# Kernel tuning notes

Measured on AMD Instinct MI355X. Metric: run time of the kernel, lower is better.

Reference implementation:

```python
import jax, jax.numpy as jnp
import numpy as np

H = 16        # num_attention_heads
KV = 4        # num_key_value_heads
HD = 128      # head_dim = hidden_size // H
ROPE_THETA = 10000.0


def _rotate_half(x):
    x1, x2 = jnp.split(x, 2, axis=-1)
    return jnp.concatenate([-x2, x1], axis=-1)


def _rope_cos_sin(seq_len, dtype):
    # inv_freq: (HD//2,), full rotary (partial_rotary_factor=1.0), attention_scaling=1.0
    inv_freq = 1.0 / (ROPE_THETA ** (jnp.arange(0, HD, 2, dtype=jnp.float32) / HD))
    pos = jnp.arange(seq_len, dtype=jnp.float32)
    freqs = pos[:, None] * inv_freq[None, :]              # (S, HD//2)
    emb = jnp.concatenate([freqs, freqs], axis=-1)        # (S, HD)
    # expansion_axis=2 -> broadcast over heads: (1, S, 1, HD)
    return (jnp.cos(emb)[None, :, None, :].astype(dtype),
            jnp.sin(emb)[None, :, None, :].astype(dtype))


def setup_inputs() -> dict:
    key = jax.random.key(0)
    k1, k2, k3, k4, k5 = jax.random.split(key, 5)
    B, S, D = 2, 2048, 2048
    hidden_states = jax.random.normal(k1, (B, S, D), dtype=jnp.float32)
    # causal mask, True = attend
    causal = jnp.tril(jnp.ones((S, S), dtype=bool))
    attention_mask = jnp.broadcast_to(causal[None, None, :, :], (B, 1, S, S))
    scale = 0.02
    Wq = jax.random.normal(k2, (D, H * HD), dtype=jnp.float32) * scale
    Wk = jax.random.normal(k3, (D, KV * HD), dtype=jnp.float32) * scale
    Wv = jax.random.normal(k4, (D, KV * HD), dtype=jnp.float32) * scale
    Wo = jax.random.normal(k5, (H, HD, D), dtype=jnp.float32) * scale
    return {"hidden_states": hidden_states, "attention_mask": attention_mask,
            "Wq": Wq, "Wk": Wk, "Wv": Wv, "Wo": Wo}


def reference(hidden_states, attention_mask, Wq, Wk, Wv, Wo):
    B, S, D = hidden_states.shape
    q = (hidden_states @ Wq).reshape(B, S, H, HD)   # bquh
    k = (hidden_states @ Wk).reshape(B, S, KV, HD)
    v = (hidden_states @ Wv).reshape(B, S, KV, HD)

    cos, sin = _rope_cos_sin(S, q.dtype)
    q = q * cos + _rotate_half(q) * sin
    k = k * cos + _rotate_half(k) * sin

    # GQA: repeat kv heads to match query heads
    groups = H // KV
    k = jnp.repeat(k, groups, axis=2)               # (B, S, H, HD)
    v = jnp.repeat(v, groups, axis=2)

    inv_norm = 1.0 / np.sqrt(HD)
    scores = jnp.einsum('bquh,bkuh->buqk', q, k) * inv_norm   # (B, H, Sq, Sk)
    scores = scores.astype(jnp.float32)
    neg = jnp.asarray(-1e9, dtype=jnp.float32)
    scores = jnp.where(attention_mask, scores, neg)
    probs = jax.nn.softmax(scores, axis=-1).astype(q.dtype)
    attn = jnp.einsum('buqk,bkuh->bquh', probs, v)             # (B, S, H, HD)
    out = jnp.einsum('bquh,uhm->bqm', attn, Wo)                # (B, S, D)
    return out
```

## Files before the change

### kernel.cpp

```cpp
#include <hip/hip_runtime.h>
#include <math.h>

namespace {

constexpr int B   = 2;
constexpr int S   = 2048;
constexpr int D   = 2048;
constexpr int NH  = 16;
constexpr int NKV = 4;
constexpr int HD  = 128;
constexpr int GRP = NH / NKV;

typedef __attribute__((ext_vector_type(8))) short  short8;
typedef __attribute__((ext_vector_type(4))) float  f32x4;
typedef unsigned short u16;

__device__ inline u16 f2bf(float f) {
    unsigned u = __float_as_uint(f);
    u = (u + 0x7FFFu + ((u >> 16) & 1u)) >> 16;
    return (u16)u;
}
__device__ inline float bf2f(u16 h) {
    return __uint_as_float((unsigned)h << 16);
}

__device__ __forceinline__ void gload_lds16(const void* g, void* l) {
    __builtin_amdgcn_global_load_lds(
        (const __attribute__((address_space(1))) unsigned int*)g,
        (__attribute__((address_space(3))) unsigned int*)l, 16, 0, 0);
}

__global__ __launch_bounds__(256)
void split_cast_kernel(const float* __restrict__ X, u16* __restrict__ H,
                       u16* __restrict__ L, int n4)
{
    const int idx = blockIdx.x * 256 + threadIdx.x;
    if (idx >= n4) return;
    const float4 v = reinterpret_cast<const float4*>(X)[idx];
    ushort4 h, l;
    h.x = f2bf(v.x); l.x = f2bf(v.x - bf2f(h.x));
    h.y = f2bf(v.y); l.y = f2bf(v.y - bf2f(h.y));
    h.z = f2bf(v.z); l.z = f2bf(v.z - bf2f(h.z));
    h.w = f2bf(v.w); l.w = f2bf(v.w - bf2f(h.w));
    reinterpret_cast<ushort4*>(H)[idx] = h;
    reinterpret_cast<ushort4*>(L)[idx] = l;
}

__global__ __launch_bounds__(256)
void wcast_t_kernel(const float* __restrict__ W, u16* __restrict__ Th,
                    u16* __restrict__ Tl, int Nw, int n_off)
{
    __shared__ u16 th[64][68];
    __shared__ u16 tl[64][68];
    const int t  = threadIdx.x;
    const int n0 = blockIdx.x * 64;
    const int k0 = blockIdx.y * 64;

#pragma unroll
    for (int i = 0; i < 4; ++i) {
        const int kr = (t >> 4) + i * 16;
        const int nc = (t & 15) * 4;
        const float4 v = *reinterpret_cast<const float4*>(
            &W[(size_t)(k0 + kr) * Nw + n0 + nc]);
        const u16 hx = f2bf(v.x), hy = f2bf(v.y), hz = f2bf(v.z), hw = f2bf(v.w);
        th[kr][nc + 0] = hx; tl[kr][nc + 0] = f2bf(v.x - bf2f(hx));
        th[kr][nc + 1] = hy; tl[kr][nc + 1] = f2bf(v.y - bf2f(hy));
        th[kr][nc + 2] = hz; tl[kr][nc + 2] = f2bf(v.z - bf2f(hz));
        th[kr][nc + 3] = hw; tl[kr][nc + 3] = f2bf(v.w - bf2f(hw));
    }
    __syncthreads();
#pragma unroll
    for (int i = 0; i < 4; ++i) {
        const int nr = (t >> 4) + i * 16;
        const int kc = (t & 15) * 4;
        ushort4 oh, ol;
        oh.x = th[kc + 0][nr]; ol.x = tl[kc + 0][nr];
        oh.y = th[kc + 1][nr]; ol.y = tl[kc + 1][nr];
        oh.z = th[kc + 2][nr]; ol.z = tl[kc + 2][nr];
        oh.w = th[kc + 3][nr]; ol.w = tl[kc + 3][nr];
        const size_t o = (size_t)(n_off + n0 + nr) * 2048 + k0 + kc;
        *reinterpret_cast<ushort4*>(&Th[o]) = oh;
        *reinterpret_cast<ushort4*>(&Tl[o]) = ol;
    }
}

__global__ __launch_bounds__(256)
void hgemm_hilo_kernel(const u16* __restrict__ Ah, const u16* __restrict__ Al,
                       const u16* __restrict__ Bth, const u16* __restrict__ Btl,
                       float* __restrict__ C, int M, int N, int K)
{
    __shared__ alignas(16) u16 AsH[4096];
    __shared__ alignas(16) u16 AsL[4096];
    __shared__ alignas(16) u16 BsH[4096];
    __shared__ alignas(16) u16 BsL[4096];

    const int t  = threadIdx.x;
    const int w  = t >> 6;
    const int l  = t & 63;
    const int lc = l & 15;
    const int kg = l >> 4;
    const int wr = w >> 1, wc = w & 1;

    const int m0 = blockIdx.y * 128;
    const int n0 = blockIdx.x * 128;

    const int srow = l >> 2;
    const int sblk = l & 3;

    f32x4 acc[4][4];
#pragma unroll
    for (int i = 0; i < 4; ++i)
#pragma unroll
        for (int j = 0; j < 4; ++j) acc[i][j] = (f32x4){0.f, 0.f, 0.f, 0.f};

    for (int k0 = 0; k0 < K; k0 += 32) {
#pragma unroll
        for (int i = 0; i < 2; ++i) {
            const int c   = i * 4 + w;
            const int row = c * 16 + srow;
            const int swb = sblk ^ ((row >> 1) & 3);
            const size_t ga = (size_t)(m0 + row) * K + k0 + swb * 8;
            const size_t gb = (size_t)(n0 + row) * K + k0 + swb * 8;
            gload_lds16(Ah  + ga, AsH + c * 512);
            gload_lds16(Al  + ga, AsL + c * 512);
            gload_lds16(Bth + gb, BsH + c * 512);
            gload_lds16(Btl + gb, BsL + c * 512);
        }
        __syncthreads();

        short8 fah[4], fal[4], fbh[4], fbl[4];
#pragma unroll
        for (int i = 0; i < 4; ++i) {
            const int ra = wr * 64 + i * 16 + lc;
            const int oa = ra * 32 + ((kg ^ ((ra >> 1) & 3)) * 8);
            fah[i] = *reinterpret_cast<const short8*>(&AsH[oa]);
            fal[i] = *reinterpret_cast<const short8*>(&AsL[oa]);
            const int rb = wc * 64 + i * 16 + lc;
            const int ob = rb * 32 + ((kg ^ ((rb >> 1) & 3)) * 8);
            fbh[i] = *reinterpret_cast<const short8*>(&BsH[ob]);
            fbl[i] = *reinterpret_cast<const short8*>(&BsL[ob]);
        }
#pragma unroll
        for (int i = 0; i < 4; ++i)
#pragma unroll
            for (int j = 0; j < 4; ++j) {
                acc[i][j] = __builtin_amdgcn_mfma_f32_16x16x32_bf16(
                    fal[i], fbh[j], acc[i][j], 0, 0, 0);
                acc[i][j] = __builtin_amdgcn_mfma_f32_16x16x32_bf16(
                    fah[i], fbl[j], acc[i][j], 0, 0, 0);
                acc[i][j] = __builtin_amdgcn_mfma_f32_16x16x32_bf16(
                    fah[i], fbh[j], acc[i][j], 0, 0, 0);
            }
        __syncthreads();
    }

#pragma unroll
    for (int i = 0; i < 4; ++i)
#pragma unroll
        for (int j = 0; j < 4; ++j)
#pragma unroll
            for (int r = 0; r < 4; ++r) {
                const int m = m0 + wr * 64 + i * 16 + kg * 4 + r;
                const int n = n0 + wc * 64 + j * 16 + lc;
                C[(size_t)m * N + n] = acc[i][j][r];
            }
}

__global__ __launch_bounds__(256)
void rope_cast_kernel(const float* __restrict__ X, int stride, int col_off,
                      u16* __restrict__ Yh, u16* __restrict__ Yl,
                      int n_heads, int total_pairs, float scale)
{
    const int idx = blockIdx.x * 256 + threadIdx.x;
    if (idx >= total_pairs) return;
    const int i    = idx & 63;
    const int rest = idx >> 6;
    const int head = rest % n_heads;
    const int row  = rest / n_heads;
    const int s    = row & (S - 1);
    const int b    = row >> 11;

    const float inv = expf(-9.2103403719761836f * (float)i * (1.0f / 64.0f));
    float sn, cs;
    sincosf((float)s * inv, &sn, &cs);

    const float* src = X + (size_t)row * stride + col_off + head * HD + i;
    const float x1 = src[0], x2 = src[64];
    const float y1 = (x1 * cs - x2 * sn) * scale;
    const float y2 = (x2 * cs + x1 * sn) * scale;

    const u16 h1 = f2bf(y1), h2 = f2bf(y2);
    const size_t o = ((size_t)(b * n_heads + head) * S + s) * HD + i;
    Yh[o] = h1;  Yh[o + 64] = h2;
    Yl[o]      = f2bf(y1 - bf2f(h1));
    Yl[o + 64] = f2bf(y2 - bf2f(h2));
}

__global__ __launch_bounds__(256)
void vcast_kernel(const float* __restrict__ V, int stride, int col_off,
                  u16* __restrict__ Yh, u16* __restrict__ Yl)
{
    __shared__ u16 th[64][68];
    __shared__ u16 tl[64][68];
    const int t  = threadIdx.x;
    const int s0 = blockIdx.x * 64, dv0 = blockIdx.y * 64;
    const int b  = blockIdx.z >> 2, u = blockIdx.z & 3;

#pragma unroll
    for (int i = 0; i < 4; ++i) {
        const int sr = (t >> 4) + i * 16;
        const int dc = (t & 15) * 4;
        const float4 v = *reinterpret_cast<const float4*>(
            &V[(size_t)(b * S + s0 + sr) * stride + col_off + u * HD + dv0 + dc]);
        const u16 hx = f2bf(v.x), hy = f2bf(v.y), hz = f2bf(v.z), hw = f2bf(v.w);
        th[sr][dc + 0] = hx; tl[sr][dc + 0] = f2bf(v.x - bf2f(hx));
        th[sr][dc + 1] = hy; tl[sr][dc + 1] = f2bf(v.y - bf2f(hy));
        th[sr][dc + 2] = hz; tl[sr][dc + 2] = f2bf(v.z - bf2f(hz));
        th[sr][dc + 3] = hw; tl[sr][dc + 3] = f2bf(v.w - bf2f(hw));
    }
    __syncthreads();
#pragma unroll
    for (int i = 0; i < 4; ++i) {
        const int dr = (t >> 4) + i * 16;
        const int sc = (t & 15) * 4;
        ushort4 oh, ol;
        oh.x = th[sc + 0][dr]; ol.x = tl[sc + 0][dr];
        oh.y = th[sc + 1][dr]; ol.y = tl[sc + 1][dr];
        oh.z = th[sc + 2][dr]; ol.z = tl[sc + 2][dr];
        oh.w = th[sc + 3][dr]; ol.w = tl[sc + 3][dr];
        const size_t o = ((size_t)(b * NKV + u) * HD + dv0 + dr) * S + s0 + sc;
        *reinterpret_cast<ushort4*>(&Yh[o]) = oh;
        *reinterpret_cast<ushort4*>(&Yl[o]) = ol;
    }
}

constexpr int QTILE = 64, KT = 32;

__global__ __launch_bounds__(256)
void flash_mfma_kernel(const u16* __restrict__ Qh, const u16* __restrict__ Ql,
                       const u16* __restrict__ Kh, const u16* __restrict__ Kl,
                       const u16* __restrict__ Vh, const u16* __restrict__ Vl,
                       u16* __restrict__ Oh, u16* __restrict__ Ol)
{
    __shared__ alignas(16) u16 smem[23552];
    u16* KsH = smem;
    u16* KsL = smem + 4096;
    u16* VtH = smem + 8192;
    u16* VtL = smem + 13312;
    u16* PH  = smem + 18432;
    u16* PL  = smem + 20992;

    const int t  = threadIdx.x;
    const int w  = t >> 6;
    const int ln = t & 63;
    const int lg = ln >> 4;
    const int lc = ln & 15;

    const int qt = (int)gridDim.x - 1 - (int)blockIdx.x;
    const int q0 = qt * QTILE;
    const int bh = blockIdx.y;
    const int b  = bh / NH, h = bh % NH, u = h / GRP;

    const size_t qbase = (size_t)(b * NH + h) * S * HD;
    const size_t kbase = (size_t)(b * NKV + u) * S * HD;
    const size_t vbase = (size_t)(b * NKV + u) * HD * S;

    {
        u16* QsH = smem;
        u16* QsL = smem + 8192;
#pragma unroll
        for (int i = 0; i < 4; ++i) {
            const int r = (t >> 4) + i * 16;
            const int blk = t & 15;
            const size_t src = qbase + (size_t)(q0 + r) * HD + blk * 8;
            const int dst = r * 128 + ((blk ^ (r & 7)) * 8);
            *reinterpret_cast<short8*>(&QsH[dst]) =
                *reinterpret_cast<const short8*>(&Qh[src]);
            *reinterpret_cast<short8*>(&QsL[dst]) =
                *reinterpret_cast<const short8*>(&Ql[src]);
        }
        __syncthreads();
    }
    short8 qah[4], qal[4];
#pragma unroll
    for (int ks = 0; ks < 4; ++ks) {
        const int qr = w * 16 + lc;
        const int off = qr * 128 + (((ks * 4 + lg) ^ (qr & 7)) * 8);
        qah[ks] = *reinterpret_cast<const short8*>(&smem[off]);
        qal[ks] = *reinterpret_cast<const short8*>(&smem[8192 + off]);
    }
    __syncthreads();

    f32x4 o[8];
#pragma unroll
    for (int i = 0; i < 8; ++i) o[i] = (f32x4){0.f, 0.f, 0.f, 0.f};
    float m_run[4] = {-1e30f, -1e30f, -1e30f, -1e30f};
    float l_run[4] = {0.f, 0.f, 0.f, 0.f};

    u16* PwH = PH + w * 640;
    u16* PwL = PL + w * 640;
    const int qw0 = q0 + w * 16;
    const int nkt = q0 / KT + 2;

    const int sr_k = t >> 4;
    const int sb_k = t & 15;
    const int sr_v = t >> 2;
    const int sb_v = t & 3;
    const int dKsw = (sb_k ^ (sr_k & 7)) * 8;
    const int dK0  = sr_k * 128 + dKsw;
    const int dK1  = (sr_k + 16) * 128 + dKsw;
    const int dV0  = sr_v * 40 + sb_v * 8;
    const int dV1  = (sr_v + 64) * 40 + sb_v * 8;

    short8 stg[8];
#define LOADTILE(K0)                                                          \
    {                                                                         \
        const size_t ksrc = kbase + (size_t)((K0) + sr_k) * HD + sb_k * 8;    \
        stg[0] = *reinterpret_cast<const short8*>(&Kh[ksrc]);                 \
        stg[1] = *reinterpret_cast<const short8*>(&Kh[ksrc + 16 * HD]);       \
        stg[2] = *reinterpret_cast<const short8*>(&Kl[ksrc]);                 \
        stg[3] = *reinterpret_cast<const short8*>(&Kl[ksrc + 16 * HD]);       \
        const size_t vsrc = vbase + (size_t)sr_v * S + (K0) + sb_v * 8;       \
        stg[4] = *reinterpret_cast<const short8*>(&Vh[vsrc]);                 \
        stg[5] = *reinterpret_cast<const short8*>(&Vh[vsrc + (size_t)64 * S]);\
        stg[6] = *reinterpret_cast<const short8*>(&Vl[vsrc]);                 \
        stg[7] = *reinterpret_cast<const short8*>(&Vl[vsrc + (size_t)64 * S]);\
    }

    LOADTILE(0);

    for (int kt = 0; kt < nkt; ++kt) {
        const int k0 = kt * KT;
        *reinterpret_cast<short8*>(&KsH[dK0]) = stg[0];
        *reinterpret_cast<short8*>(&KsH[dK1]) = stg[1];
        *reinterpret_cast<short8*>(&KsL[dK0]) = stg[2];
        *reinterpret_cast<short8*>(&KsL[dK1]) = stg[3];
        *reinterpret_cast<short8*>(&VtH[dV0]) = stg[4];
        *reinterpret_cast<short8*>(&VtH[dV1]) = stg[5];
        *reinterpret_cast<short8*>(&VtL[dV0]) = stg[6];
        *reinterpret_cast<short8*>(&VtL[dV1]) = stg[7];
        __syncthreads();

        if (kt + 1 < nkt) LOADTILE(k0 + KT);

        if (k0 <= qw0 + 15) {
            f32x4 a0 = {0.f, 0.f, 0.f, 0.f}, a1 = {0.f, 0.f, 0.f, 0.f};
            __builtin_amdgcn_s_setprio(1);
#pragma unroll
            for (int ks = 0; ks < 4; ++ks) {
                const int r0 = lc, r1 = 16 + lc;
                const int o0b = r0 * 128 + (((ks * 4 + lg) ^ (r0 & 7)) * 8);
                const int o1b = r1 * 128 + (((ks * 4 + lg) ^ (r1 & 7)) * 8);
                const short8 kb0h = *reinterpret_cast<const short8*>(&KsH[o0b]);
                const short8 kb0l = *reinterpret_cast<const short8*>(&KsL[o0b]);
                const short8 kb1h = *reinterpret_cast<const short8*>(&KsH[o1b]);
                const short8 kb1l = *reinterpret_cast<const short8*>(&KsL[o1b]);
                a0 = __builtin_amdgcn_mfma_f32_16x16x32_bf16(qal[ks], kb0h, a0, 0, 0, 0);
                a0 = __builtin_amdgcn_mfma_f32_16x16x32_bf16(qah[ks], kb0l, a0, 0, 0, 0);
                a0 = __builtin_amdgcn_mfma_f32_16x16x32_bf16(qah[ks], kb0h, a0, 0, 0, 0);
                a1 = __builtin_amdgcn_mfma_f32_16x16x32_bf16(qal[ks], kb1h, a1, 0, 0, 0);
                a1 = __builtin_amdgcn_mfma_f32_16x16x32_bf16(qah[ks], kb1l, a1, 0, 0, 0);
                a1 = __builtin_amdgcn_mfma_f32_16x16x32_bf16(qah[ks], kb1h, a1, 0, 0, 0);
            }
            __builtin_amdgcn_s_setprio(0);

            float s0v[4], s1v[4], mx[4];
            const bool need_mask = (k0 + KT - 1 > qw0);
#pragma unroll
            for (int r = 0; r < 4; ++r) {
                float s0 = a0[r], s1 = a1[r];
                const int qg = qw0 + lg * 4 + r;
                if (need_mask) {
                    if (k0 + lc > qg)      s0 = -1e30f;
                    if (k0 + 16 + lc > qg) s1 = -1e30f;
                }
                s0v[r] = s0; s1v[r] = s1;
                mx[r] = fmaxf(s0, s1);
            }
#pragma unroll
            for (int off = 1; off < 16; off <<= 1)
#pragma unroll
                for (int r = 0; r < 4; ++r)
                    mx[r] = fmaxf(mx[r], __shfl_xor(mx[r], off, 64));

            bool grow = false;
#pragma unroll
            for (int r = 0; r < 4; ++r) grow = grow || (mx[r] > m_run[r] + 8.0f);
            const bool resc_needed = __any((int)grow);

            float mn[4], rsc[4];
#pragma unroll
            for (int r = 0; r < 4; ++r) {
                mn[r]  = resc_needed ? fmaxf(m_run[r], mx[r]) : m_run[r];
                rsc[r] = resc_needed ? __expf(m_run[r] - mn[r]) : 1.0f;
            }
            float p0[4], p1[4], rs[4];
#pragma unroll
            for (int r = 0; r < 4; ++r) {
                p0[r] = __expf(s0v[r] - mn[r]);
                p1[r] = __expf(s1v[r] - mn[r]);
                rs[r] = p0[r] + p1[r];
            }
#pragma unroll
            for (int off = 1; off < 16; off <<= 1)
#pragma unroll
                for (int r = 0; r < 4; ++r)
                    rs[r] += __shfl_xor(rs[r], off, 64);
#pragma unroll
            for (int r = 0; r < 4; ++r) {
                l_run[r] = l_run[r] * rsc[r] + rs[r];
                m_run[r] = mn[r];
            }
            if (resc_needed) {
#pragma unroll
                for (int nt = 0; nt < 8; ++nt)
#pragma unroll
                    for (int r = 0; r < 4; ++r) o[nt][r] *= rsc[r];
            }
#pragma unroll
            for (int r = 0; r < 4; ++r) {
                const u16 p0h = f2bf(p0[r]);
                const u16 p1h = f2bf(p1[r]);
                const int row = (lg * 4 + r) * 40;
                PwH[row + lc]      = p0h;
                PwH[row + 16 + lc] = p1h;
                PwL[row + lc]      = f2bf(p0[r] - bf2f(p0h));
                PwL[row + 16 + lc] = f2bf(p1[r] - bf2f(p1h));
            }
            asm volatile("s_waitcnt lgkmcnt(0)" ::: "memory");

            const short8 pah = *reinterpret_cast<const short8*>(&PwH[lc * 40 + lg * 8]);
            const short8 pal = *reinterpret_cast<const short8*>(&PwL[lc * 40 + lg * 8]);
            __builtin_amdgcn_s_setprio(1);
#pragma unroll
            for (int nt = 0; nt < 8; ++nt) {
                const int dvo = (nt * 16 + lc) * 40 + lg * 8;
                const short8 vbh = *reinterpret_cast<const short8*>(&VtH[dvo]);
                const short8 vbl = *reinterpret_cast<const short8*>(&VtL[dvo]);
                o[nt] = __builtin_amdgcn_mfma_f32_16x16x32_bf16(pal, vbh, o[nt], 0, 0, 0);
                o[nt] = __builtin_amdgcn_mfma_f32_16x16x32_bf16(pah, vbl, o[nt], 0, 0, 0);
                o[nt] = __builtin_amdgcn_mfma_f32_16x16x32_bf16(pah, vbh, o[nt], 0, 0, 0);
            }
            __builtin_amdgcn_s_setprio(0);
        }
        __syncthreads();
    }
#undef LOADTILE

    float invl[4];
#pragma unroll
    for (int r = 0; r < 4; ++r) invl[r] = 1.f / l_run[r];
#pragma unroll
    for (int nt = 0; nt < 8; ++nt) {
#pragma unroll
        for (int r = 0; r < 4; ++r) {
            const float v = o[nt][r] * invl[r];
            const size_t off =
                (size_t)(b * S + qw0 + lg * 4 + r) * (NH * HD) + h * HD + nt * 16 + lc;
            const u16 hv = f2bf(v);
            Oh[off] = hv;
            Ol[off] = f2bf(v - bf2f(hv));
        }
    }
}

}

extern "C" void kernel_launch(void* const* d_in, const int* in_sizes, int n_in,
                              void* d_out, int out_size, void* d_ws, size_t ws_size,
                              hipStream_t stream)
{
    const float* hidden = (const float*)d_in[0];
    const float* Wq = (const float*)d_in[2];
    const float* Wk = (const float*)d_in[3];
    const float* Wv = (const float*)d_in[4];
    const float* Wo = (const float*)d_in[5];
    float* out = (float*)d_out;

    char* wsb = (char*)d_ws;
    u16*   hid_hi  = (u16*)(wsb);
    u16*   hid_lo  = (u16*)(wsb + 16777216);
    float* qkv_f   = (float*)(wsb + 33554432);
    u16*   k_hi    = (u16*)(wsb + 83886080);
    u16*   k_lo    = (u16*)(wsb + 88080384);
    u16*   v_hi    = (u16*)(wsb + 92274688);
    u16*   v_lo    = (u16*)(wsb + 96468992);
    u16*   wT_hi   = (u16*)(wsb + 100663296);
    u16*   wT_lo   = (u16*)(wsb + 113246208);
    u16* q_hi    = hid_hi;
    u16* q_lo    = hid_lo;
    u16* attn_hi = (u16*)(wsb + 33554432);
    u16* attn_lo = (u16*)(wsb + 50331648);
    u16* woT_hi  = wT_hi;
    u16* woT_lo  = wT_lo;

    const dim3 blk(256);

    split_cast_kernel<<<dim3(8192), blk, 0, stream>>>(hidden, hid_hi, hid_lo, 2097152);
    wcast_t_kernel<<<dim3(32, 32), blk, 0, stream>>>(Wq, wT_hi, wT_lo, 2048, 0);
    wcast_t_kernel<<<dim3(8, 32),  blk, 0, stream>>>(Wk, wT_hi, wT_lo, 512, 2048);
    wcast_t_kernel<<<dim3(8, 32),  blk, 0, stream>>>(Wv, wT_hi, wT_lo, 512, 2560);
    hgemm_hilo_kernel<<<dim3(24, 32), blk, 0, stream>>>(
        hid_hi, hid_lo, wT_hi, wT_lo, qkv_f, 4096, 3072, 2048);
    wcast_t_kernel<<<dim3(32, 32), blk, 0, stream>>>(Wo, woT_hi, woT_lo, 2048, 0);
    const int qpairs = 4096 * NH * 64;
    const int kpairs = 4096 * NKV * 64;
    rope_cast_kernel<<<dim3(qpairs / 256), blk, 0, stream>>>(
        qkv_f, 3072, 0, q_hi, q_lo, NH, qpairs, 0.08838834764831845f);
    rope_cast_kernel<<<dim3(kpairs / 256), blk, 0, stream>>>(
        qkv_f, 3072, 2048, k_hi, k_lo, NKV, kpairs, 1.0f);
    vcast_kernel<<<dim3(32, 2, 8), blk, 0, stream>>>(
        qkv_f, 3072, 2560, v_hi, v_lo);
    flash_mfma_kernel<<<dim3(S / QTILE, B * NH), blk, 0, stream>>>(
        q_hi, q_lo, k_hi, k_lo, v_hi, v_lo, attn_hi, attn_lo);
    hgemm_hilo_kernel<<<dim3(16, 32), blk, 0, stream>>>(
        attn_hi, attn_lo, woT_hi, woT_lo, out, 4096, 2048, 2048);
}
```

Before: 797.6 us.

## Transpose QK^T MFMA so each lane holds one query row's scores

Swaps the MFMA operand order in the score product so S^T is computed and each lane owns a single query row with four key columns. Row max and row sum then need two cross-lane shuffles instead of eight, and the running max and sum become scalars per lane. The probability tile is written to LDS with packed 64-bit stores instead of scalar 16-bit stores. The rescale factors and the final normalizer are redistributed to the output layout with extra shuffles, which adds a little work on the rescale path.

```diff
diff --git a/kernel.cpp b/kernel.cpp
--- a/kernel.cpp
+++ b/kernel.cpp
@@ -294,8 +294,7 @@
     f32x4 o[8];
 #pragma unroll
     for (int i = 0; i < 8; ++i) o[i] = (f32x4){0.f, 0.f, 0.f, 0.f};
-    float m_run[4] = {-1e30f, -1e30f, -1e30f, -1e30f};
-    float l_run[4] = {0.f, 0.f, 0.f, 0.f};
+    float m_run = -1e30f, l_run = 0.f;
 
     u16* PwH = PH + w * 640;
     u16* PwL = PL + w * 640;
@@ -355,77 +354,82 @@
                 const short8 kb0l = *reinterpret_cast<const short8*>(&KsL[o0b]);
                 const short8 kb1h = *reinterpret_cast<const short8*>(&KsH[o1b]);
                 const short8 kb1l = *reinterpret_cast<const short8*>(&KsL[o1b]);
-                a0 = __builtin_amdgcn_mfma_f32_16x16x32_bf16(qal[ks], kb0h, a0, 0, 0, 0);
-                a0 = __builtin_amdgcn_mfma_f32_16x16x32_bf16(qah[ks], kb0l, a0, 0, 0, 0);
-                a0 = __builtin_amdgcn_mfma_f32_16x16x32_bf16(qah[ks], kb0h, a0, 0, 0, 0);
-                a1 = __builtin_amdgcn_mfma_f32_16x16x32_bf16(qal[ks], kb1h, a1, 0, 0, 0);
-                a1 = __builtin_amdgcn_mfma_f32_16x16x32_bf16(qah[ks], kb1l, a1, 0, 0, 0);
-                a1 = __builtin_amdgcn_mfma_f32_16x16x32_bf16(qah[ks], kb1h, a1, 0, 0, 0);
+                a0 = __builtin_amdgcn_mfma_f32_16x16x32_bf16(kb0h, qal[ks], a0, 0, 0, 0);
+                a0 = __builtin_amdgcn_mfma_f32_16x16x32_bf16(kb0l, qah[ks], a0, 0, 0, 0);
+                a0 = __builtin_amdgcn_mfma_f32_16x16x32_bf16(kb0h, qah[ks], a0, 0, 0, 0);
+                a1 = __builtin_amdgcn_mfma_f32_16x16x32_bf16(kb1h, qal[ks], a1, 0, 0, 0);
+                a1 = __builtin_amdgcn_mfma_f32_16x16x32_bf16(kb1l, qah[ks], a1, 0, 0, 0);
+                a1 = __builtin_amdgcn_mfma_f32_16x16x32_bf16(kb1h, qah[ks], a1, 0, 0, 0);
             }
             __builtin_amdgcn_s_setprio(0);
 
-            float s0v[4], s1v[4], mx[4];
-            const bool need_mask = (k0 + KT - 1 > qw0);
+            const int qg = qw0 + lc;
+            const int kb = k0 + lg * 4;
+            if (k0 + KT - 1 > qw0) {
+#pragma unroll
+                for (int r = 0; r < 4; ++r) {
+                    if (kb + r > qg)      a0[r] = -1e30f;
+                    if (kb + 16 + r > qg) a1[r] = -1e30f;
+                }
+            }
+
+            float mx = fmaxf(fmaxf(fmaxf(a0[0], a0[1]), fmaxf(a0[2], a0[3])),
+                             fmaxf(fmaxf(a1[0], a1[1]), fmaxf(a1[2], a1[3])));
+            mx = fmaxf(mx, __shfl_xor(mx, 16, 64));
+            mx = fmaxf(mx, __shfl_xor(mx, 32, 64));
+
+            const bool resc_needed = __any((int)(mx > m_run + 8.0f));
+            float mn = m_run, rsc = 1.0f;
+            if (resc_needed) {
+                mn  = fmaxf(m_run, mx);
+                rsc = __expf(m_run - mn);
+            }
+
+            float p0[4], p1[4];
+            float rs = 0.f;
 #pragma unroll
             for (int r = 0; r < 4; ++r) {
-                float s0 = a0[r], s1 = a1[r];
-                const int qg = qw0 + lg * 4 + r;
-                if (need_mask) {
-                    if (k0 + lc > qg)      s0 = -1e30f;
-                    if (k0 + 16 + lc > qg) s1 = -1e30f;
+                p0[r] = __expf(a0[r] - mn);
+                p1[r] = __expf(a1[r] - mn);
+                rs += p0[r] + p1[r];
+            }
+            rs += __shfl_xor(rs, 16, 64);
+            rs += __shfl_xor(rs, 32, 64);
+            l_run = l_run * rsc + rs;
+            m_run = mn;
+
+            if (resc_needed) {
+                float rr[4];
+#pragma unroll
+                for (int r = 0; r < 4; ++r)
+                    rr[r] = __shfl(rsc, lg * 4 + r, 64);
+#pragma unroll
+                for (int nt = 0; nt < 8; ++nt)
+#pragma unroll
+                    for (int r = 0; r < 4; ++r) o[nt][r] *= rr[r];
+            }
+
+            {
+                u16 h0[4], h1[4], l0[4], l1[4];
+#pragma unroll
+                for (int r = 0; r < 4; ++r) {
+                    h0[r] = f2bf(p0[r]); l0[r] = f2bf(p0[r] - bf2f(h0[r]));
+                    h1[r] = f2bf(p1[r]); l1[r] = f2bf(p1[r] - bf2f(h1[r]));
                 }
-                s0v[r] = s0; s1v[r] = s1;
-                mx[r] = fmaxf(s0, s1);
-            }
-#pragma unroll
-            for (int off = 1; off < 16; off <<= 1)
-#pragma unroll
-                for (int r = 0; r < 4; ++r)
-                    mx[r] = fmaxf(mx[r], __shfl_xor(mx[r], off, 64));
-
-            bool grow = false;
-#pragma unroll
-            for (int r = 0; r < 4; ++r) grow = grow || (mx[r] > m_run[r] + 8.0f);
-            const bool resc_needed = __any((int)grow);
-
-            float mn[4], rsc[4];
-#pragma unroll
-            for (int r = 0; r < 4; ++r) {
-                mn[r]  = resc_needed ? fmaxf(m_run[r], mx[r]) : m_run[r];
-                rsc[r] = resc_needed ? __expf(m_run[r] - mn[r]) : 1.0f;
-            }
-            float p0[4], p1[4], rs[4];
-#pragma unroll
-            for (int r = 0; r < 4; ++r) {
-                p0[r] = __expf(s0v[r] - mn[r]);
-                p1[r] = __expf(s1v[r] - mn[r]);
-                rs[r] = p0[r] + p1[r];
-            }
-#pragma unroll
-            for (int off = 1; off < 16; off <<= 1)
-#pragma unroll
-                for (int r = 0; r < 4; ++r)
-                    rs[r] += __shfl_xor(rs[r], off, 64);
-#pragma unroll
-            for (int r = 0; r < 4; ++r) {
-                l_run[r] = l_run[r] * rsc[r] + rs[r];
-                m_run[r] = mn[r];
-            }
-            if (resc_needed) {
-#pragma unroll
-                for (int nt = 0; nt < 8; ++nt)
-#pragma unroll
-                    for (int r = 0; r < 4; ++r) o[nt][r] *= rsc[r];
-            }
-#pragma unroll
-            for (int r = 0; r < 4; ++r) {
-                const u16 p0h = f2bf(p0[r]);
-                const u16 p1h = f2bf(p1[r]);
-                const int row = (lg * 4 + r) * 40;
-                PwH[row + lc]      = p0h;
-                PwH[row + 16 + lc] = p1h;
-                PwL[row + lc]      = f2bf(p0[r] - bf2f(p0h));
-                PwL[row + 16 + lc] = f2bf(p1[r] - bf2f(p1h));
+                const int base = lc * 40 + lg * 4;
+                uint2 v;
+                v.x = (unsigned)h0[0] | ((unsigned)h0[1] << 16);
+                v.y = (unsigned)h0[2] | ((unsigned)h0[3] << 16);
+                *reinterpret_cast<uint2*>(&PwH[base]) = v;
+                v.x = (unsigned)h1[0] | ((unsigned)h1[1] << 16);
+                v.y = (unsigned)h1[2] | ((unsigned)h1[3] << 16);
+                *reinterpret_cast<uint2*>(&PwH[base + 16]) = v;
+                v.x = (unsigned)l0[0] | ((unsigned)l0[1] << 16);
+                v.y = (unsigned)l0[2] | ((unsigned)l0[3] << 16);
+                *reinterpret_cast<uint2*>(&PwL[base]) = v;
+                v.x = (unsigned)l1[0] | ((unsigned)l1[1] << 16);
+                v.y = (unsigned)l1[2] | ((unsigned)l1[3] << 16);
+                *reinterpret_cast<uint2*>(&PwL[base + 16]) = v;
             }
             asm volatile("s_waitcnt lgkmcnt(0)" ::: "memory");
 
@@ -447,9 +451,10 @@
     }
 #undef LOADTILE
 
+    const float linv = 1.f / l_run;
     float invl[4];
 #pragma unroll
-    for (int r = 0; r < 4; ++r) invl[r] = 1.f / l_run[r];
+    for (int r = 0; r < 4; ++r) invl[r] = __shfl(linv, lg * 4 + r, 64);
 #pragma unroll
     for (int nt = 0; nt < 8; ++nt) {
 #pragma unroll
```

New measurement: 716.3 us. 1.11x faster.
